# Performance work log

Measured on AMD Instinct MI355X. Metric: run time of the kernel, lower is better.

## Reference

```python
import jax, jax.numpy as jnp
import numpy as np

N_NODES = 100_000
N_EDGES = 1_600_000
HEADS = 3
DIMS = [6, 8, 16, 32]  # in -> conv1 -> conv2 -> conv3 out_feats


def _edge_gat(x, ef, src, dst, W, We, al, ar, ae, b, n_nodes):
    """DGL EdgeGATConv: edge feats modulate attention logits; messages are alpha * W h_src."""
    H, D = al.shape
    ft = (x @ W.T).reshape(n_nodes, H, D)          # [N,H,D] projected node feats
    fe = (ef @ We.T).reshape(-1, H, D)             # [E,H,D] projected edge feats
    el = jnp.sum(ft * al, axis=-1)                 # [N,H]
    er = jnp.sum(ft * ar, axis=-1)                 # [N,H]
    ee = jnp.sum(fe * ae, axis=-1)                 # [E,H]
    e = jax.nn.leaky_relu(el[src] + er[dst] + ee, 0.2)  # [E,H] (DGL default slope 0.2)
    # segment softmax over incoming edges of each dst node
    m = jax.ops.segment_max(e, dst, num_segments=n_nodes)
    m = jnp.where(jnp.isfinite(m), m, 0.0)         # zero-in-degree nodes
    ex = jnp.exp(e - m[dst])
    denom = jax.ops.segment_sum(ex, dst, num_segments=n_nodes)
    a = ex / jnp.maximum(denom[dst], 1e-9)         # [E,H]
    msg = a[:, :, None] * ft[src]                  # [E,H,D]
    out = jax.ops.segment_sum(msg, dst, num_segments=n_nodes)  # [N,H,D]
    return out + b.reshape(1, H, D)


def setup_inputs() -> dict:
    key = jax.random.key(0)
    ks = jax.random.split(key, 32)
    d = {
        "node_feats": jax.random.normal(ks[0], (N_NODES, DIMS[0]), jnp.float32),
        "edge_feats": jax.random.uniform(ks[1], (N_EDGES, 1), jnp.float32),
        "src": jax.random.randint(ks[2], (N_EDGES,), 0, N_NODES, jnp.int32),
        "dst": jax.random.randint(ks[3], (N_EDGES,), 0, N_NODES, jnp.int32),
    }
    ki = 4
    for i in range(3):
        fin, fout = DIMS[i], DIMS[i + 1]
        s = 1.0 / np.sqrt(fin)
        d[f"W{i+1}"] = jax.random.normal(ks[ki], (HEADS * fout, fin), jnp.float32) * s; ki += 1
        d[f"We{i+1}"] = jax.random.normal(ks[ki], (HEADS * fout, 1), jnp.float32); ki += 1
        d[f"al{i+1}"] = jax.random.normal(ks[ki], (HEADS, fout), jnp.float32) * 0.1; ki += 1
        d[f"ar{i+1}"] = jax.random.normal(ks[ki], (HEADS, fout), jnp.float32) * 0.1; ki += 1
        d[f"ae{i+1}"] = jax.random.normal(ks[ki], (HEADS, fout), jnp.float32) * 0.1; ki += 1
        d[f"b{i+1}"] = jnp.zeros((HEADS * fout,), jnp.float32)
    for name, (fo, fi) in [("l1", (16, 32)), ("l2", (4, 16)), ("l3", (1, 4)), ("l4", (1, HEADS))]:
        s = 1.0 / np.sqrt(fi)
        d[name + "w"] = jax.random.uniform(ks[ki], (fo, fi), jnp.float32, -s, s); ki += 1
        d[name + "b"] = jax.random.uniform(ks[ki], (fo,), jnp.float32, -s, s); ki += 1
    return d


def reference(node_feats, edge_feats, src, dst,
              W1, We1, al1, ar1, ae1, b1,
              W2, We2, al2, ar2, ae2, b2,
              W3, We3, al3, ar3, ae3, b3,
              l1w, l1b, l2w, l2b, l3w, l3b, l4w, l4b):
    n = node_feats.shape[0]
    h1 = _edge_gat(node_feats, edge_feats, src, dst, W1, We1, al1, ar1, ae1, b1, n)  # [N,3,8]
    h2 = _edge_gat(h1.mean(axis=1), edge_feats, src, dst, W2, We2, al2, ar2, ae2, b2, n)  # [N,3,16]
    h3 = _edge_gat(h2.mean(axis=1), edge_feats, src, dst, W3, We3, al3, ar3, ae3, b3, n)  # [N,3,32]
    # per-(node,head) MLP head: 32 -> 16 -> 4 -> 1
    x = jax.nn.leaky_relu(h3 @ l1w.T + l1b, 0.01)
    x = jax.nn.leaky_relu(x @ l2w.T + l2b, 0.01)
    x = x @ l3w.T + l3b                            # [N,3,1]
    feats = x.reshape(n, -1) @ l4w.T + l4b         # [N,1] combine heads
    return jnp.max(feats, axis=0)                  # [1]
```

## Files before the change

### kernel.cpp

```cpp
#include <hip/hip_runtime.h>
#include <hip/hip_bf16.h>
#include <hip/hip_fp16.h>

#define HEADS 3

union HU { uint4 u; __half2 h[4]; };

__global__ void prep_ce_kernel(const float* __restrict__ We1, const float* __restrict__ ae1,
                               const float* __restrict__ We2, const float* __restrict__ ae2,
                               const float* __restrict__ We3, const float* __restrict__ ae3,
                               float* __restrict__ ce) {
    int t = threadIdx.x;
    if (t >= 9) return;
    int l = t / 3, h = t % 3;
    const float* We = (l == 0) ? We1 : (l == 1) ? We2 : We3;
    const float* ae = (l == 0) ? ae1 : (l == 1) ? ae2 : ae3;
    int D = (l == 0) ? 8 : (l == 1) ? 16 : 32;
    float s = 0.f;
    for (int d = 0; d < D; d++) s += We[h * D + d] * ae[h * D + d];
    ce[t] = s;
}

__global__ void hist_kernel(const int* __restrict__ dst, int* __restrict__ deg, int E) {
    int tid = blockIdx.x * blockDim.x + threadIdx.x;
    if (tid < E) atomicAdd(&deg[dst[tid]], 1);
}

#define SCAN_BLK 1024
__global__ void scan1_kernel(const int* __restrict__ deg, int* __restrict__ row_ptr,
                             int* __restrict__ partials, int N) {
    __shared__ int sm[SCAN_BLK];
    int t = threadIdx.x;
    int g = blockIdx.x * SCAN_BLK + t;
    int v = (g < N) ? deg[g] : 0;
    sm[t] = v;
    __syncthreads();
    for (int off = 1; off < SCAN_BLK; off <<= 1) {
        int x = (t >= off) ? sm[t - off] : 0;
        __syncthreads();
        sm[t] += x;
        __syncthreads();
    }
    if (g < N) row_ptr[g] = sm[t] - v;
    if (t == SCAN_BLK - 1) partials[blockIdx.x] = sm[t];
}

__global__ void scan2_kernel(int* __restrict__ partials, int NB) {
    __shared__ int sm[128];
    int t = threadIdx.x;
    int v = (t < NB) ? partials[t] : 0;
    sm[t] = v;
    __syncthreads();
    for (int off = 1; off < 128; off <<= 1) {
        int x = (t >= off) ? sm[t - off] : 0;
        __syncthreads();
        sm[t] += x;
        __syncthreads();
    }
    if (t < NB) partials[t] = sm[t] - v;
    if (t == 127) partials[NB] = sm[127];
}

__global__ void scan3_kernel(int* __restrict__ row_ptr, const int* __restrict__ partials,
                             int N, int NB) {
    int g = blockIdx.x * SCAN_BLK + threadIdx.x;
    if (g < N) row_ptr[g] += partials[blockIdx.x];
    if (blockIdx.x == 0 && threadIdx.x == 0) row_ptr[N] = partials[NB];
}

__global__ void scatter_kernel(const int* __restrict__ src, const int* __restrict__ dst,
                               const float* __restrict__ ef, const int* __restrict__ row_ptr,
                               int* __restrict__ cnt, int2* __restrict__ erec, int E) {
    int tid = blockIdx.x * blockDim.x + threadIdx.x;
    if (tid >= E) return;
    int d = dst[tid];
    int pos = row_ptr[d] + atomicAdd(&cnt[d], 1);
    int2 r;
    r.x = src[tid];
    r.y = __float_as_int(ef[tid]);
    erec[pos] = r;
}

template <int FIN, int D, bool MEAN_PREV>
__launch_bounds__(256)
__global__ void node_kernel(const float* __restrict__ xin,
                            const float* __restrict__ W,
                            const float* __restrict__ al,
                            const float* __restrict__ ar,
                            __half* __restrict__ ft,
                            float* __restrict__ el, float* __restrict__ er,
                            int N) {
    int tid = blockIdx.x * blockDim.x + threadIdx.x;
    if (tid >= N * HEADS) return;
    int n = tid / HEADS, h = tid % HEADS;
    float x[FIN];
    if (MEAN_PREV) {
        #pragma unroll
        for (int k = 0; k < FIN; k++)
            x[k] = (xin[(n * HEADS + 0) * FIN + k] +
                    xin[(n * HEADS + 1) * FIN + k] +
                    xin[(n * HEADS + 2) * FIN + k]) * (1.0f / 3.0f);
    } else {
        #pragma unroll
        for (int k = 0; k < FIN; k++) x[k] = xin[n * FIN + k];
    }
    float fv[D];
    float e_l = 0.f, e_r = 0.f;
    #pragma unroll
    for (int d = 0; d < D; d++) {
        const float* wr = &W[(h * D + d) * FIN];
        float f = 0.f;
        #pragma unroll
        for (int k = 0; k < FIN; k++) f += x[k] * wr[k];
        fv[d] = f;
        e_l += f * al[h * D + d];
        e_r += f * ar[h * D + d];
    }
    uint4* dst16 = (uint4*)(ft + (size_t)tid * D);
    #pragma unroll
    for (int q = 0; q < D / 8; q++) {
        HU u;
        #pragma unroll
        for (int j = 0; j < 4; j++)
            u.h[j] = __floats2half2_rn(fv[q * 8 + 2 * j], fv[q * 8 + 2 * j + 1]);
        dst16[q] = u.u;
    }
    el[tid] = e_l;
    er[tid] = e_r;
}

template <int D>
__launch_bounds__(256)
__global__ void agg_kernel(const int* __restrict__ row_ptr, const int2* __restrict__ erec,
                           const __half* __restrict__ ft,
                           const float* __restrict__ el, const float* __restrict__ er,
                           const float* __restrict__ ce,
                           const float* __restrict__ b,
                           float* __restrict__ out,
                           int NH) {
    int unit = blockIdx.x * blockDim.x + threadIdx.x;
    if (unit >= NH) return;
    int n = unit / HEADS, h = unit - n * HEADS;
    int beg = row_ptr[n], end = row_ptr[n + 1];

    float ern = er[unit];
    float ceh = ce[h];
    float m = -3.0e38f, ssum = 0.f;
    float msg[D];
    #pragma unroll
    for (int d = 0; d < D; d++) msg[d] = 0.f;

    int e = beg;
    for (; e + 3 < end; e += 4) {
        int2 r0 = erec[e + 0], r1 = erec[e + 1], r2 = erec[e + 2], r3 = erec[e + 3];
        float v0 = el[r0.x * HEADS + h] + ern + __int_as_float(r0.y) * ceh;
        float v1 = el[r1.x * HEADS + h] + ern + __int_as_float(r1.y) * ceh;
        float v2 = el[r2.x * HEADS + h] + ern + __int_as_float(r2.y) * ceh;
        float v3 = el[r3.x * HEADS + h] + ern + __int_as_float(r3.y) * ceh;
        v0 = v0 > 0.f ? v0 : 0.2f * v0;
        v1 = v1 > 0.f ? v1 : 0.2f * v1;
        v2 = v2 > 0.f ? v2 : 0.2f * v2;
        v3 = v3 > 0.f ? v3 : 0.2f * v3;
        float cm = fmaxf(fmaxf(v0, v1), fmaxf(v2, v3));
        if (cm > m) {
            float sc = __expf(m - cm);
            ssum *= sc;
            #pragma unroll
            for (int d = 0; d < D; d++) msg[d] *= sc;
            m = cm;
        }
        float x0 = __expf(v0 - m), x1 = __expf(v1 - m);
        float x2 = __expf(v2 - m), x3 = __expf(v3 - m);
        ssum += (x0 + x1) + (x2 + x3);
        const uint4* f0 = (const uint4*)(ft + ((size_t)r0.x * HEADS + h) * D);
        const uint4* f1 = (const uint4*)(ft + ((size_t)r1.x * HEADS + h) * D);
        const uint4* f2 = (const uint4*)(ft + ((size_t)r2.x * HEADS + h) * D);
        const uint4* f3 = (const uint4*)(ft + ((size_t)r3.x * HEADS + h) * D);
        #pragma unroll
        for (int q = 0; q < D / 8; q++) {
            HU a0, a1, a2, a3;
            a0.u = f0[q]; a1.u = f1[q]; a2.u = f2[q]; a3.u = f3[q];
            #pragma unroll
            for (int j = 0; j < 4; j++) {
                float2 p0 = __half22float2(a0.h[j]);
                float2 p1 = __half22float2(a1.h[j]);
                float2 p2 = __half22float2(a2.h[j]);
                float2 p3 = __half22float2(a3.h[j]);
                msg[q * 8 + 2 * j + 0] += x0 * p0.x + x1 * p1.x + x2 * p2.x + x3 * p3.x;
                msg[q * 8 + 2 * j + 1] += x0 * p0.y + x1 * p1.y + x2 * p2.y + x3 * p3.y;
            }
        }
    }
    for (; e < end; e++) {
        int2 r = erec[e];
        float v = el[r.x * HEADS + h] + ern + __int_as_float(r.y) * ceh;
        v = v > 0.f ? v : 0.2f * v;
        if (v > m) {
            float sc = __expf(m - v);
            ssum *= sc;
            #pragma unroll
            for (int d = 0; d < D; d++) msg[d] *= sc;
            m = v;
        }
        float x = __expf(v - m);
        ssum += x;
        const uint4* fr = (const uint4*)(ft + ((size_t)r.x * HEADS + h) * D);
        #pragma unroll
        for (int q = 0; q < D / 8; q++) {
            HU a; a.u = fr[q];
            #pragma unroll
            for (int j = 0; j < 4; j++) {
                float2 p = __half22float2(a.h[j]);
                msg[q * 8 + 2 * j + 0] += x * p.x;
                msg[q * 8 + 2 * j + 1] += x * p.y;
            }
        }
    }

    float inv = 1.0f / fmaxf(ssum, 1e-9f);
    float4* ob = (float4*)(out + (size_t)unit * D);
    #pragma unroll
    for (int d = 0; d < D; d += 4) {
        float4 v;
        v.x = msg[d + 0] * inv + b[h * D + d + 0];
        v.y = msg[d + 1] * inv + b[h * D + d + 1];
        v.z = msg[d + 2] * inv + b[h * D + d + 2];
        v.w = msg[d + 3] * inv + b[h * D + d + 3];
        ob[d / 4] = v;
    }
}

__global__ void mlp_max_kernel(const float* __restrict__ h3,
                               const float* __restrict__ l1w, const float* __restrict__ l1b,
                               const float* __restrict__ l2w, const float* __restrict__ l2b,
                               const float* __restrict__ l3w, const float* __restrict__ l3b,
                               const float* __restrict__ l4w, const float* __restrict__ l4b,
                               unsigned int* __restrict__ maxkey, int N) {
    int tid = blockIdx.x * blockDim.x + threadIdx.x;
    float feat = -3.0e38f;
    if (tid < N) {
        float acc = l4b[0];
        #pragma unroll
        for (int h = 0; h < HEADS; h++) {
            const float4* vp = (const float4*)&h3[((size_t)tid * HEADS + h) * 32];
            float v[32];
            #pragma unroll
            for (int q = 0; q < 8; q++) {
                float4 t = vp[q];
                v[q * 4 + 0] = t.x; v[q * 4 + 1] = t.y; v[q * 4 + 2] = t.z; v[q * 4 + 3] = t.w;
            }
            float y1[16];
            #pragma unroll
            for (int i = 0; i < 16; i++) {
                float s = l1b[i];
                const float* w = &l1w[i * 32];
                #pragma unroll
                for (int k = 0; k < 32; k++) s += v[k] * w[k];
                y1[i] = s > 0.f ? s : 0.01f * s;
            }
            float y2[4];
            #pragma unroll
            for (int i = 0; i < 4; i++) {
                float s = l2b[i];
                const float* w = &l2w[i * 16];
                #pragma unroll
                for (int k = 0; k < 16; k++) s += y1[k] * w[k];
                y2[i] = s > 0.f ? s : 0.01f * s;
            }
            float y3 = l3b[0];
            #pragma unroll
            for (int k = 0; k < 4; k++) y3 += y2[k] * l3w[k];
            acc += y3 * l4w[h];
        }
        feat = acc;
    }
    #pragma unroll
    for (int off = 32; off > 0; off >>= 1)
        feat = fmaxf(feat, __shfl_down(feat, off));
    if ((threadIdx.x & 63) == 0) {
        unsigned int u = __float_as_uint(feat);
        unsigned int key = (u & 0x80000000u) ? ~u : (u | 0x80000000u);
        atomicMax(maxkey, key);
    }
}

__global__ void finalize_kernel(const unsigned int* __restrict__ maxkey, float* __restrict__ out) {
    unsigned int key = *maxkey;
    unsigned int u = (key & 0x80000000u) ? (key & 0x7FFFFFFFu) : ~key;
    out[0] = __uint_as_float(u);
}

extern "C" void kernel_launch(void* const* d_in, const int* in_sizes, int n_in,
                              void* d_out, int out_size, void* d_ws, size_t ws_size,
                              hipStream_t stream) {
    const float* node_feats = (const float*)d_in[0];
    const float* edge_feats = (const float*)d_in[1];
    const int* src = (const int*)d_in[2];
    const int* dst = (const int*)d_in[3];
    const float* W1  = (const float*)d_in[4];
    const float* We1 = (const float*)d_in[5];
    const float* al1 = (const float*)d_in[6];
    const float* ar1 = (const float*)d_in[7];
    const float* ae1 = (const float*)d_in[8];
    const float* b1  = (const float*)d_in[9];
    const float* W2  = (const float*)d_in[10];
    const float* We2 = (const float*)d_in[11];
    const float* al2 = (const float*)d_in[12];
    const float* ar2 = (const float*)d_in[13];
    const float* ae2 = (const float*)d_in[14];
    const float* b2  = (const float*)d_in[15];
    const float* W3  = (const float*)d_in[16];
    const float* We3 = (const float*)d_in[17];
    const float* al3 = (const float*)d_in[18];
    const float* ar3 = (const float*)d_in[19];
    const float* ae3 = (const float*)d_in[20];
    const float* b3  = (const float*)d_in[21];
    const float* l1w = (const float*)d_in[22];
    const float* l1b = (const float*)d_in[23];
    const float* l2w = (const float*)d_in[24];
    const float* l2b = (const float*)d_in[25];
    const float* l3w = (const float*)d_in[26];
    const float* l3b = (const float*)d_in[27];
    const float* l4w = (const float*)d_in[28];
    const float* l4b = (const float*)d_in[29];

    const int N = in_sizes[0] / 6;
    const int E = in_sizes[2];
    const int NB = (N + SCAN_BLK - 1) / SCAN_BLK;

    char* ws = (char*)d_ws;
    size_t off = 0;
    auto alloc = [&](size_t bytes) -> void* {
        void* p = ws + off;
        off = (off + bytes + 255) & ~(size_t)255;
        return p;
    };
    int* deg            = (int*)alloc((size_t)N * 4);
    int* cnt            = (int*)alloc((size_t)N * 4);
    unsigned int* mkey  = (unsigned int*)alloc(4);
    size_t zero_bytes   = off;
    int* row_ptr        = (int*)alloc((size_t)(N + 1) * 4);
    int* partials       = (int*)alloc((size_t)(NB + 1) * 4);
    int2* erec          = (int2*)alloc((size_t)E * 8);
    __half* ft          = (__half*)alloc((size_t)N * 96 * 2);
    float* outb         = (float*)alloc((size_t)N * 96 * 4);
    float* el           = (float*)alloc((size_t)N * 3 * 4);
    float* er           = (float*)alloc((size_t)N * 3 * 4);
    float* ce           = (float*)alloc(9 * 4);

    hipMemsetAsync(d_ws, 0, zero_bytes, stream);

    prep_ce_kernel<<<1, 16, 0, stream>>>(We1, ae1, We2, ae2, We3, ae3, ce);
    hist_kernel<<<(E + 255) / 256, 256, 0, stream>>>(dst, deg, E);
    scan1_kernel<<<NB, SCAN_BLK, 0, stream>>>(deg, row_ptr, partials, N);
    scan2_kernel<<<1, 128, 0, stream>>>(partials, NB);
    scan3_kernel<<<NB, SCAN_BLK, 0, stream>>>(row_ptr, partials, N, NB);
    scatter_kernel<<<(E + 255) / 256, 256, 0, stream>>>(src, dst, edge_feats, row_ptr, cnt,
                                                        erec, E);

    const int NH = N * HEADS;
    const int gb = (NH + 255) / 256;

    node_kernel<6, 8, false><<<gb, 256, 0, stream>>>(node_feats, W1, al1, ar1, ft, el, er, N);
    agg_kernel<8><<<gb, 256, 0, stream>>>(row_ptr, erec, ft, el, er, ce + 0, b1, outb, NH);
    node_kernel<8, 16, true><<<gb, 256, 0, stream>>>(outb, W2, al2, ar2, ft, el, er, N);
    agg_kernel<16><<<gb, 256, 0, stream>>>(row_ptr, erec, ft, el, er, ce + 3, b2, outb, NH);
    node_kernel<16, 32, true><<<gb, 256, 0, stream>>>(outb, W3, al3, ar3, ft, el, er, N);
    agg_kernel<32><<<gb, 256, 0, stream>>>(row_ptr, erec, ft, el, er, ce + 6, b3, outb, NH);

    mlp_max_kernel<<<(N + 255) / 256, 256, 0, stream>>>(outb, l1w, l1b, l2w, l2b, l3w, l3b,
                                                        l4w, l4b, mkey, N);
    finalize_kernel<<<1, 1, 0, stream>>>(mkey, (float*)d_out);
}
```

Before: 523.9 us.

## Split each node-head's incoming edges across two lanes with shuffle-merged softmax

The aggregation kernel now gives each (node, head) pair two lanes. Each lane processes half of the node's incoming edges with its own online softmax. The partial max, sum and message vectors are merged through wavefront shuffles, and each lane writes half of the output. This roughly doubles the thread count and halves the serial per-thread edge loop, aiming for more memory-level parallelism. The cost is extra shuffles of D accumulators and 4 idle lanes per 64-lane wavefront.

```diff
diff --git a/kernel.cpp b/kernel.cpp
--- a/kernel.cpp
+++ b/kernel.cpp
@@ -137,96 +137,123 @@
                            const float* __restrict__ ce,
                            const float* __restrict__ b,
                            float* __restrict__ out,
-                           int NH) {
-    int unit = blockIdx.x * blockDim.x + threadIdx.x;
-    if (unit >= NH) return;
-    int n = unit / HEADS, h = unit - n * HEADS;
-    int beg = row_ptr[n], end = row_ptr[n + 1];
-
-    float ern = er[unit];
-    float ceh = ce[h];
+                           int N) {
+    int w = threadIdx.x >> 6;
+    int l = threadIdx.x & 63;
+    int wl = l / 6;
+    int rem = l - wl * 6;
+    int s = rem >= 3 ? 1 : 0;
+    int h = rem - s * 3;
+    int n = (blockIdx.x * 4 + w) * 10 + wl;
+    bool active = (wl < 10) && (n < N);
+
     float m = -3.0e38f, ssum = 0.f;
     float msg[D];
     #pragma unroll
     for (int d = 0; d < D; d++) msg[d] = 0.f;
-
-    int e = beg;
-    for (; e + 3 < end; e += 4) {
-        int2 r0 = erec[e + 0], r1 = erec[e + 1], r2 = erec[e + 2], r3 = erec[e + 3];
-        float v0 = el[r0.x * HEADS + h] + ern + __int_as_float(r0.y) * ceh;
-        float v1 = el[r1.x * HEADS + h] + ern + __int_as_float(r1.y) * ceh;
-        float v2 = el[r2.x * HEADS + h] + ern + __int_as_float(r2.y) * ceh;
-        float v3 = el[r3.x * HEADS + h] + ern + __int_as_float(r3.y) * ceh;
-        v0 = v0 > 0.f ? v0 : 0.2f * v0;
-        v1 = v1 > 0.f ? v1 : 0.2f * v1;
-        v2 = v2 > 0.f ? v2 : 0.2f * v2;
-        v3 = v3 > 0.f ? v3 : 0.2f * v3;
-        float cm = fmaxf(fmaxf(v0, v1), fmaxf(v2, v3));
-        if (cm > m) {
-            float sc = __expf(m - cm);
-            ssum *= sc;
-            #pragma unroll
-            for (int d = 0; d < D; d++) msg[d] *= sc;
-            m = cm;
+    int unit = n * HEADS + h;
+    float ceh = ce[h];
+
+    if (active) {
+        int beg = row_ptr[n], end = row_ptr[n + 1];
+        int cnt = end - beg;
+        int half = (cnt + 1) >> 1;
+        int es = beg + s * half;
+        int ee = s ? end : (beg + half);
+        float ern = er[unit];
+
+        int e = es;
+        for (; e + 3 < ee; e += 4) {
+            int2 r0 = erec[e + 0], r1 = erec[e + 1], r2 = erec[e + 2], r3 = erec[e + 3];
+            float v0 = el[r0.x * HEADS + h] + ern + __int_as_float(r0.y) * ceh;
+            float v1 = el[r1.x * HEADS + h] + ern + __int_as_float(r1.y) * ceh;
+            float v2 = el[r2.x * HEADS + h] + ern + __int_as_float(r2.y) * ceh;
+            float v3 = el[r3.x * HEADS + h] + ern + __int_as_float(r3.y) * ceh;
+            v0 = v0 > 0.f ? v0 : 0.2f * v0;
+            v1 = v1 > 0.f ? v1 : 0.2f * v1;
+            v2 = v2 > 0.f ? v2 : 0.2f * v2;
+            v3 = v3 > 0.f ? v3 : 0.2f * v3;
+            float cm = fmaxf(fmaxf(v0, v1), fmaxf(v2, v3));
+            if (cm > m) {
+                float sc = __expf(m - cm);
+                ssum *= sc;
+                #pragma unroll
+                for (int d = 0; d < D; d++) msg[d] *= sc;
+                m = cm;
+            }
+            float x0 = __expf(v0 - m), x1 = __expf(v1 - m);
+            float x2 = __expf(v2 - m), x3 = __expf(v3 - m);
+            ssum += (x0 + x1) + (x2 + x3);
+            const uint4* f0 = (const uint4*)(ft + ((size_t)r0.x * HEADS + h) * D);
+            const uint4* f1 = (const uint4*)(ft + ((size_t)r1.x * HEADS + h) * D);
+            const uint4* f2 = (const uint4*)(ft + ((size_t)r2.x * HEADS + h) * D);
+            const uint4* f3 = (const uint4*)(ft + ((size_t)r3.x * HEADS + h) * D);
+            #pragma unroll
+            for (int q = 0; q < D / 8; q++) {
+                HU a0, a1, a2, a3;
+                a0.u = f0[q]; a1.u = f1[q]; a2.u = f2[q]; a3.u = f3[q];
+                #pragma unroll
+                for (int j = 0; j < 4; j++) {
+                    float2 p0 = __half22float2(a0.h[j]);
+                    float2 p1 = __half22float2(a1.h[j]);
+                    float2 p2 = __half22float2(a2.h[j]);
+                    float2 p3 = __half22float2(a3.h[j]);
+                    msg[q * 8 + 2 * j + 0] += x0 * p0.x + x1 * p1.x + x2 * p2.x + x3 * p3.x;
+                    msg[q * 8 + 2 * j + 1] += x0 * p0.y + x1 * p1.y + x2 * p2.y + x3 * p3.y;
+                }
+            }
         }
-        float x0 = __expf(v0 - m), x1 = __expf(v1 - m);
-        float x2 = __expf(v2 - m), x3 = __expf(v3 - m);
-        ssum += (x0 + x1) + (x2 + x3);
-        const uint4* f0 = (const uint4*)(ft + ((size_t)r0.x * HEADS + h) * D);
-        const uint4* f1 = (const uint4*)(ft + ((size_t)r1.x * HEADS + h) * D);
-        const uint4* f2 = (const uint4*)(ft + ((size_t)r2.x * HEADS + h) * D);
-        const uint4* f3 = (const uint4*)(ft + ((size_t)r3.x * HEADS + h) * D);
-        #pragma unroll
-        for (int q = 0; q < D / 8; q++) {
-            HU a0, a1, a2, a3;
-            a0.u = f0[q]; a1.u = f1[q]; a2.u = f2[q]; a3.u = f3[q];
-            #pragma unroll
-            for (int j = 0; j < 4; j++) {
-                float2 p0 = __half22float2(a0.h[j]);
-                float2 p1 = __half22float2(a1.h[j]);
-                float2 p2 = __half22float2(a2.h[j]);
-                float2 p3 = __half22float2(a3.h[j]);
-                msg[q * 8 + 2 * j + 0] += x0 * p0.x + x1 * p1.x + x2 * p2.x + x3 * p3.x;
-                msg[q * 8 + 2 * j + 1] += x0 * p0.y + x1 * p1.y + x2 * p2.y + x3 * p3.y;
+        for (; e < ee; e++) {
+            int2 r = erec[e];
+            float v = el[r.x * HEADS + h] + ern + __int_as_float(r.y) * ceh;
+            v = v > 0.f ? v : 0.2f * v;
+            if (v > m) {
+                float sc = __expf(m - v);
+                ssum *= sc;
+                #pragma unroll
+                for (int d = 0; d < D; d++) msg[d] *= sc;
+                m = v;
+            }
+            float x = __expf(v - m);
+            ssum += x;
+            const uint4* fr = (const uint4*)(ft + ((size_t)r.x * HEADS + h) * D);
+            #pragma unroll
+            for (int q = 0; q < D / 8; q++) {
+                HU a; a.u = fr[q];
+                #pragma unroll
+                for (int j = 0; j < 4; j++) {
+                    float2 p = __half22float2(a.h[j]);
+                    msg[q * 8 + 2 * j + 0] += x * p.x;
+                    msg[q * 8 + 2 * j + 1] += x * p.y;
+                }
             }
         }
     }
-    for (; e < end; e++) {
-        int2 r = erec[e];
-        float v = el[r.x * HEADS + h] + ern + __int_as_float(r.y) * ceh;
-        v = v > 0.f ? v : 0.2f * v;
-        if (v > m) {
-            float sc = __expf(m - v);
-            ssum *= sc;
-            #pragma unroll
-            for (int d = 0; d < D; d++) msg[d] *= sc;
-            m = v;
+
+    int pl = (s ? (l - 3) : (l + 3)) & 63;
+    float om = __shfl(m, pl);
+    float osum = __shfl(ssum, pl);
+    float M = fmaxf(m, om);
+    float sA = __expf(m - M);
+    float sB = __expf(om - M);
+    float tot = ssum * sA + osum * sB;
+    float inv = 1.0f / fmaxf(tot, 1e-9f);
+    #pragma unroll
+    for (int d = 0; d < D; d++)
+        msg[d] = msg[d] * sA + __shfl(msg[d], pl) * sB;
+
+    if (active) {
+        int lo = s * (D / 2);
+        float* ob = out + (size_t)unit * D + lo;
+        #pragma unroll
+        for (int d = 0; d < D / 2; d += 4) {
+            float4 v;
+            v.x = msg[lo + d + 0] * inv + b[h * D + lo + d + 0];
+            v.y = msg[lo + d + 1] * inv + b[h * D + lo + d + 1];
+            v.z = msg[lo + d + 2] * inv + b[h * D + lo + d + 2];
+            v.w = msg[lo + d + 3] * inv + b[h * D + lo + d + 3];
+            *(float4*)(ob + d) = v;
         }
-        float x = __expf(v - m);
-        ssum += x;
-        const uint4* fr = (const uint4*)(ft + ((size_t)r.x * HEADS + h) * D);
-        #pragma unroll
-        for (int q = 0; q < D / 8; q++) {
-            HU a; a.u = fr[q];
-            #pragma unroll
-            for (int j = 0; j < 4; j++) {
-                float2 p = __half22float2(a.h[j]);
-                msg[q * 8 + 2 * j + 0] += x * p.x;
-                msg[q * 8 + 2 * j + 1] += x * p.y;
-            }
-        }
-    }
-
-    float inv = 1.0f / fmaxf(ssum, 1e-9f);
-    float4* ob = (float4*)(out + (size_t)unit * D);
-    #pragma unroll
-    for (int d = 0; d < D; d += 4) {
-        float4 v;
-        v.x = msg[d + 0] * inv + b[h * D + d + 0];
-        v.y = msg[d + 1] * inv + b[h * D + d + 1];
-        v.z = msg[d + 2] * inv + b[h * D + d + 2];
-        v.w = msg[d + 3] * inv + b[h * D + d + 3];
-        ob[d / 4] = v;
     }
 }
 
@@ -360,13 +387,14 @@
 
     const int NH = N * HEADS;
     const int gb = (NH + 255) / 256;
+    const int gb_agg = (N + 39) / 40;
 
     node_kernel<6, 8, false><<<gb, 256, 0, stream>>>(node_feats, W1, al1, ar1, ft, el, er, N);
-    agg_kernel<8><<<gb, 256, 0, stream>>>(row_ptr, erec, ft, el, er, ce + 0, b1, outb, NH);
+    agg_kernel<8><<<gb_agg, 256, 0, stream>>>(row_ptr, erec, ft, el, er, ce + 0, b1, outb, N);
     node_kernel<8, 16, true><<<gb, 256, 0, stream>>>(outb, W2, al2, ar2, ft, el, er, N);
-    agg_kernel<16><<<gb, 256, 0, stream>>>(row_ptr, erec, ft, el, er, ce + 3, b2, outb, NH);
+    agg_kernel<16><<<gb_agg, 256, 0, stream>>>(row_ptr, erec, ft, el, er, ce + 3, b2, outb, N);
     node_kernel<16, 32, true><<<gb, 256, 0, stream>>>(outb, W3, al3, ar3, ft, el, er, N);
-    agg_kernel<32><<<gb, 256, 0, stream>>>(row_ptr, erec, ft, el, er, ce + 6, b3, outb, NH);
+    agg_kernel<32><<<gb_agg, 256, 0, stream>>>(row_ptr, erec, ft, el, er, ce + 6, b3, outb, N);
 
     mlp_max_kernel<<<(N + 255) / 256, 256, 0, stream>>>(outb, l1w, l1b, l2w, l2b, l3w, l3b,
                                                         l4w, l4b, mkey, N);
```

Result: no change. 520.9 us (-0.6%).
